# Kernel optimization log

Hardware: AMD Instinct MI355X
Metric: run time of the kernel (lower is better)

The kernel has to match this reference:

```python
import jax, jax.numpy as jnp
import numpy as np
import math

B, L, S, T = 16, 128, 128, 128
QDIM, FDIM, HID, ODIM = 512, 512, 512, 512

def setup_inputs() -> dict:
    key = jax.random.key(0)
    ks = jax.random.split(key, 9)
    sc = 0.02
    return {
        "query": jax.random.normal(ks[0], (B, L, QDIM), dtype=jnp.float32),
        "src": jax.random.normal(ks[1], (B, S, FDIM), dtype=jnp.float32),
        "trg": jax.random.normal(ks[2], (B, T, FDIM), dtype=jnp.float32),
        "Wq": jax.random.normal(ks[3], (QDIM, HID), dtype=jnp.float32) * sc,
        "bq": jnp.zeros((HID,), dtype=jnp.float32),
        "Ws": jax.random.normal(ks[4], (FDIM, HID), dtype=jnp.float32) * sc,
        "bs": jnp.zeros((HID,), dtype=jnp.float32),
        "Wo": jax.random.normal(ks[5], (FDIM * 2 + QDIM, ODIM), dtype=jnp.float32) * sc,
        "bo": jnp.zeros((ODIM,), dtype=jnp.float32),
    }

def reference(query, src, trg, Wq, bq, Ws, bs, Wo, bo):
    b, l, _ = query.shape
    s = src.shape[1]
    t = trg.shape[1]
    q = query @ Wq + bq            # [b,l,h]
    s_key = src @ Ws + bs          # [b,s,h]  (src_linear == trg_linear, shared weights)
    t_key = trg @ Ws + bs          # [b,t,h]
    # trilinear scores: [b,l,s,t]
    weight = jnp.einsum('blk,bsk,btk->blst', q, s_key, t_key) / math.sqrt(HID)
    weight = jax.nn.softmax(weight.reshape(b, l, s * t), axis=-1).reshape(b, l, s, t)
    s_ctx = jnp.einsum('blst,bsf->blf', weight, src)
    t_ctx = jnp.einsum('blst,btf->blf', weight, trg)
    x = jnp.concatenate((query, s_ctx, t_ctx), axis=-1)
    return x @ Wo + bo
```

## Files before the change

kernel.cpp:

```cpp
#include <hip/hip_runtime.h>
#include <hip/hip_bf16.h>

typedef __attribute__((ext_vector_type(8))) short short8;
typedef __attribute__((ext_vector_type(4))) short short4v;
typedef __attribute__((ext_vector_type(4))) float f32x4;
typedef __attribute__((ext_vector_type(8))) _Float16 half8;

#define DEVINL static __device__ __forceinline__

constexpr float SCORE_SCALE = 0.063758977414048896f;

typedef const __attribute__((address_space(1))) void gv_t;
typedef __attribute__((address_space(3))) void lv_t;
DEVINL void gload16(const void* g, void* l) {
  __builtin_amdgcn_global_load_lds((gv_t*)g, (lv_t*)l, 16, 0, 0);
}

#define SWZ_ADD(v, pat)                                                    \
  v += __int_as_float(__builtin_amdgcn_ds_swizzle(__float_as_int(v), pat))

template <int M, int N>
DEVINL void gemm16(const _Float16* A, const _Float16* B, int K, int lda, int ldb,
                   _Float16* ldsA, _Float16* ldsB, f32x4 acc[M / 32][N / 32])
{
  const int tid = threadIdx.x, lane = tid & 63;
  const int wr = (tid >> 7) & 1, wc = (tid >> 6) & 1;
  constexpr int MA = M / 32, NB = N / 32;
  int aoff[MA], boff[NB];
#pragma unroll
  for (int i = 0; i < MA; ++i) {
    const int ci = tid + i * 256, row = ci >> 3, c = ci & 7;
    aoff[i] = row * lda + ((c ^ (row & 7)) << 3);
  }
#pragma unroll
  for (int i = 0; i < NB; ++i) {
    const int ci = tid + i * 256, row = ci >> 3, c = ci & 7;
    boff[i] = row * ldb + ((c ^ (row & 7)) << 3);
  }
#define G16STAGE(cur, kk)                                                        \
  {                                                                              \
    _Pragma("unroll")                                                            \
    for (int i = 0; i < MA; ++i)                                                 \
      gload16(A + aoff[i] + (kk), ldsA + (cur) * (M * 64) + (tid + i * 256) * 8);\
    _Pragma("unroll")                                                            \
    for (int i = 0; i < NB; ++i)                                                 \
      gload16(B + boff[i] + (kk), ldsB + (cur) * (N * 64) + (tid + i * 256) * 8);\
  }
  G16STAGE(0, 0);
  __syncthreads();
  for (int kk = 0; kk < K; kk += 64) {
    const int cur = (kk >> 6) & 1;
    if (kk + 64 < K) G16STAGE(cur ^ 1, kk + 64);
    const _Float16* bA = ldsA + cur * (M * 64);
    const _Float16* bB = ldsB + cur * (N * 64);
#pragma unroll
    for (int s = 0; s < 2; ++s) {
      const int cg2 = s * 4 + (lane >> 4);
      half8 afr[MA], bfr[NB];
#pragma unroll
      for (int mi = 0; mi < MA; ++mi) {
        const int r = wr * (M / 2) + mi * 16 + (lane & 15);
        afr[mi] = *(const half8*)(bA + r * 64 + ((cg2 ^ (r & 7)) << 3));
      }
#pragma unroll
      for (int ni = 0; ni < NB; ++ni) {
        const int r = wc * (N / 2) + ni * 16 + (lane & 15);
        bfr[ni] = *(const half8*)(bB + r * 64 + ((cg2 ^ (r & 7)) << 3));
      }
#pragma unroll
      for (int mi = 0; mi < MA; ++mi)
#pragma unroll
        for (int ni = 0; ni < NB; ++ni)
          acc[mi][ni] = __builtin_amdgcn_mfma_f32_16x16x32_f16(afr[mi], bfr[ni], acc[mi][ni], 0, 0, 0);
    }
    __syncthreads();
  }
#undef G16STAGE
}

__global__ __launch_bounds__(256) void k_prep(
    const float* __restrict__ query, const float* __restrict__ src,
    const float* __restrict__ trg,
    const float* __restrict__ Wq, const float* __restrict__ Ws,
    const float* __restrict__ Wo,
    _Float16* __restrict__ qx, _Float16* __restrict__ srch,
    _Float16* __restrict__ trgh,
    _Float16* __restrict__ WqT, _Float16* __restrict__ WsT,
    _Float16* __restrict__ WoT)
{
  __shared__ float t[32][33];
  const int id = blockIdx.x, tid = threadIdx.x;
  if (id < 1536) {
    const int z = id >> 9;
    const int idx8 = (((id & 511) << 8) + tid) * 8;
    const float* in = (z == 0) ? query : (z == 1) ? src : trg;
    float4 va = *(const float4*)(in + idx8);
    float4 vb = *(const float4*)(in + idx8 + 4);
    half8 h;
    h[0] = (_Float16)va.x; h[1] = (_Float16)va.y;
    h[2] = (_Float16)va.z; h[3] = (_Float16)va.w;
    h[4] = (_Float16)vb.x; h[5] = (_Float16)vb.y;
    h[6] = (_Float16)vb.z; h[7] = (_Float16)vb.w;
    _Float16* o = (z == 0) ? qx : (z == 1) ? srch : trgh;
    *(half8*)(o + idx8) = h;
    return;
  }
  const float* in; _Float16* out; int KK, NN, bx, by;
  if (id < 1792)      { const int u = id - 1536; in = Wq; out = WqT; KK = 512;  NN = 512; bx = u & 15; by = u >> 4; }
  else if (id < 2048) { const int u = id - 1792; in = Ws; out = WsT; KK = 512;  NN = 512; bx = u & 15; by = u >> 4; }
  else                { const int u = id - 2048; in = Wo; out = WoT; KK = 1536; NN = 512; bx = u & 15; by = u >> 4; }
  const int tx = tid & 31, ty = tid >> 5;
  const int k0 = by * 32, n0 = bx * 32;
#pragma unroll
  for (int i = 0; i < 4; ++i)
    t[ty + i * 8][tx] = in[(size_t)(k0 + ty + i * 8) * NN + n0 + tx];
  __syncthreads();
#pragma unroll
  for (int i = 0; i < 4; ++i)
    out[(size_t)(n0 + ty + i * 8) * KK + k0 + tx] = (_Float16)t[tx][ty + i * 8];
}

__global__ __launch_bounds__(256) void k_proj(
    const _Float16* __restrict__ qx, const _Float16* __restrict__ srch,
    const _Float16* __restrict__ trgh,
    const _Float16* __restrict__ WqT, const _Float16* __restrict__ WsT,
    const _Float16* __restrict__ WoT,
    const float* __restrict__ bq, const float* __restrict__ bs,
    _Float16* __restrict__ qh, _Float16* __restrict__ skh,
    _Float16* __restrict__ tkh, _Float16* __restrict__ P2)
{
  __shared__ __align__(16) _Float16 lds[24576];
  const int id = blockIdx.x;
  const int tid = threadIdx.x, lane = tid & 63;
  const int wr = (tid >> 7) & 1, wc = (tid >> 6) & 1;
  const int r0 = wr * 32 + ((lane >> 4) << 2);
  const int c0 = wc * 64 + (lane & 15);

  f32x4 acc[2][4] = {};

  if (id < 384) {
    const int z = id >> 7, u = id & 127;
    const int bcol = (u & 3) * 128, brow = (u >> 2) * 64;
    const _Float16* A = (z == 0) ? qx : (z == 1) ? srch : trgh;
    const _Float16* BT = (z == 0) ? WqT : WsT;
    const float* bias = (z == 0) ? bq : bs;
    gemm16<64, 128>(A + (size_t)brow * 512, BT + (size_t)bcol * 512,
                    512, 512, 512, lds, lds + 8192, acc);
#pragma unroll
    for (int mi = 0; mi < 2; ++mi)
#pragma unroll
      for (int ni = 0; ni < 4; ++ni) {
        const int col = bcol + c0 + ni * 16;
        const float bv = bias[col];
#pragma unroll
        for (int r = 0; r < 4; ++r) {
          const int row = brow + r0 + mi * 16 + r;
          const float v = acc[mi][ni][r] + bv;
          if (z == 0)      qh[(size_t)row * 512 + col] = (_Float16)(v * SCORE_SCALE);
          else if (z == 1) skh[(size_t)row * 512 + col] = (_Float16)v;
          else             tkh[(size_t)row * 512 + col] = (_Float16)v;
        }
      }
  } else {
    const int side = (id - 384) >> 7, u = (id - 384) & 127;
    const int b = u >> 3, brow = (u & 7) * 64;
    const _Float16* A = WoT + (size_t)brow * 1536 + 512 + side * 512;
    const _Float16* B = (side ? trgh : srch) + (size_t)b * 65536;
    gemm16<64, 128>(A, B, 512, 1536, 512, lds, lds + 8192, acc);
    _Float16* P = P2 + (size_t)b * 131072 + side * 128;
#pragma unroll
    for (int mi = 0; mi < 2; ++mi)
#pragma unroll
      for (int ni = 0; ni < 4; ++ni) {
        const int col = c0 + ni * 16;
#pragma unroll
        for (int r = 0; r < 4; ++r) {
          const int row = brow + r0 + mi * 16 + r;
          P[(size_t)row * 256 + col] = (_Float16)acc[mi][ni][r];
        }
      }
  }
}

__global__ __launch_bounds__(512, 4) void k_score(
    const _Float16* __restrict__ qh, const _Float16* __restrict__ skh,
    const _Float16* __restrict__ tkh,
    _Float16* __restrict__ wct2)
{
  __shared__ __align__(16) char pool[51200];
  _Float16* qlds = (_Float16*)(pool + 49152);
  float* wsp   = (float*)(pool);
  float* wtp   = (float*)(pool + 4096);
  float* wfin  = (float*)(pool + 8192);
  float* denom = (float*)(pool + 12288);

  const int raw = blockIdx.x;
  const int swz = (raw & 7) * 128 + (raw >> 3);
  const int b = swz >> 6, l0 = (swz & 63) * 2;

  const int tid = threadIdx.x, lane = tid & 63, wid = tid >> 6;
  const int l = wid >> 2, qs = (wid >> 1) & 1, qt = wid & 1;
  const int cg = lane >> 4;
  const int ln = lane & 15;
  const _Float16* skb = skh + (size_t)b * 65536;
  const _Float16* tkb = tkh + (size_t)b * 65536;

  int soff;
  {
    const int row = tid >> 2, c = tid & 3;
    soff = row * 512 + ((c ^ ((row >> 1) & 3)) << 3);
  }

  if (tid < 256) {
    const int li = tid >> 7, e = (tid & 127) * 4;
    *(short4v*)(qlds + li * 512 + e) =
        *(const short4v*)(qh + (size_t)(b * 128 + l0 + li) * 512 + e);
  }

  const int rbase_s = (qs * 64 + ln) * 64;
  const int rbase_t = (qt * 64 + ln) * 64;
  const int sw = (cg ^ ((ln >> 1) & 3)) << 4;

#define KSTAGE(dstbuf, kt)                                                  \
  {                                                                         \
    gload16(skb + soff + (kt) * 32, (dstbuf) + tid * 16);                   \
    gload16(tkb + soff + (kt) * 32, (dstbuf) + 8192 + tid * 16);            \
  }

  f32x4 acc[4][4] = {};
  char* bufA = pool;
  char* bufB = pool + 16384;
  char* bufC = pool + 32768;
  KSTAGE(bufA, 0);
  KSTAGE(bufB, 1);
  asm volatile("s_waitcnt vmcnt(0) lgkmcnt(0)" ::: "memory");
  __builtin_amdgcn_sched_barrier(0);
  __builtin_amdgcn_s_barrier();
  __builtin_amdgcn_sched_barrier(0);

  for (int it = 0; it < 16; ++it) {
    if (it < 14) KSTAGE(bufC, it + 2);
    half8 qv = *(const half8*)(qlds + l * 512 + it * 32 + cg * 8);
    half8 sfr[4], tfr[4];
#pragma unroll
    for (int mi = 0; mi < 4; ++mi)
      sfr[mi] = *(const half8*)(bufA + rbase_s + mi * 1024 + sw);
#pragma unroll
    for (int ni = 0; ni < 4; ++ni)
      tfr[ni] = *(const half8*)(bufA + 8192 + rbase_t + ni * 1024 + sw);
    __builtin_amdgcn_s_setprio(1);
#pragma unroll
    for (int mi = 0; mi < 4; ++mi) {
      half8 a = sfr[mi] * qv;
#pragma unroll
      for (int ni = 0; ni < 4; ++ni)
        acc[mi][ni] = __builtin_amdgcn_mfma_f32_16x16x32_f16(a, tfr[ni], acc[mi][ni], 0, 0, 0);
    }
    __builtin_amdgcn_s_setprio(0);
    if (it < 14) { asm volatile("s_waitcnt vmcnt(2)" ::: "memory"); }
    else         { asm volatile("s_waitcnt vmcnt(0)" ::: "memory"); }
    __builtin_amdgcn_sched_barrier(0);
    __builtin_amdgcn_s_barrier();
    __builtin_amdgcn_sched_barrier(0);
    char* t_ = bufA; bufA = bufB; bufB = bufC; bufC = t_;
  }
#undef KSTAGE

#pragma unroll
  for (int mi = 0; mi < 4; ++mi)
#pragma unroll
    for (int ni = 0; ni < 4; ++ni)
#pragma unroll
      for (int r = 0; r < 4; ++r)
        acc[mi][ni][r] = exp2f(acc[mi][ni][r]);

#pragma unroll
  for (int mi = 0; mi < 4; ++mi)
#pragma unroll
    for (int r = 0; r < 4; ++r) {
      float v = acc[mi][0][r] + acc[mi][1][r] + acc[mi][2][r] + acc[mi][3][r];
      SWZ_ADD(v, 0x041F);
      SWZ_ADD(v, 0x081F);
      SWZ_ADD(v, 0x101F);
      SWZ_ADD(v, 0x201F);
      if ((lane & 15) == 0)
        wsp[(l * 2 + qt) * 128 + qs * 64 + mi * 16 + (lane >> 4) * 4 + r] = v;
    }
#pragma unroll
  for (int ni = 0; ni < 4; ++ni) {
    float v = 0.f;
#pragma unroll
    for (int mi = 0; mi < 4; ++mi)
#pragma unroll
      for (int r = 0; r < 4; ++r) v += acc[mi][ni][r];
    SWZ_ADD(v, 0x401F);
    v += __shfl_xor(v, 32);
    if (lane < 16) wtp[(l * 2 + qs) * 128 + qt * 64 + ni * 16 + lane] = v;
  }
  __syncthreads();

  if (tid < 256) {
    const int li = tid >> 7, idx = tid & 127;
    wfin[(li * 2 + 0) * 128 + idx] =
        wsp[(li * 2 + 0) * 128 + idx] + wsp[(li * 2 + 1) * 128 + idx];
  } else {
    const int u = tid - 256, li = u >> 7, idx = u & 127;
    wfin[(li * 2 + 1) * 128 + idx] =
        wtp[(li * 2 + 0) * 128 + idx] + wtp[(li * 2 + 1) * 128 + idx];
  }
  __syncthreads();
  if (wid < 2) {
    float v = wfin[wid * 256 + lane] + wfin[wid * 256 + lane + 64];
#pragma unroll
    for (int off = 32; off >= 1; off >>= 1) v += __shfl_xor(v, off);
    if (lane == 0) denom[wid] = v;
  }
  __syncthreads();
  const float inv0 = 1.0f / denom[0], inv1 = 1.0f / denom[1];

  if (tid < 256) {
    const int li = tid >> 7, idx = tid & 127;
    const float inv = li ? inv1 : inv0;
    wct2[((size_t)(b * 128 + l0 + li)) * 256 + idx] =
        (_Float16)(wfin[li * 256 + idx] * inv);
  } else {
    const int u = tid - 256, li = u >> 7, idx = u & 127;
    const float inv = li ? inv1 : inv0;
    wct2[((size_t)(b * 128 + l0 + li)) * 256 + 128 + idx] =
        (_Float16)(wfin[li * 256 + 128 + idx] * inv);
  }
}

__global__ __launch_bounds__(256) void k_final(
    const _Float16* __restrict__ qx, const _Float16* __restrict__ WoT,
    const _Float16* __restrict__ wct2, const _Float16* __restrict__ P2,
    const float* __restrict__ bo, float* __restrict__ out)
{
  __shared__ __align__(16) _Float16 lds[16384];
  const int brow = blockIdx.y * 64, bcol = blockIdx.x * 64;
  const int b = blockIdx.y >> 1;

  f32x4 acc[2][2] = {};
  gemm16<64, 64>(qx + (size_t)brow * 512, WoT + (size_t)bcol * 1536,
                 512, 512, 1536, lds, lds + 8192, acc);
  gemm16<64, 64>(wct2 + (size_t)brow * 256,
                 P2 + (size_t)b * 131072 + (size_t)bcol * 256,
                 256, 256, 256, lds, lds + 8192, acc);

  const int tid = threadIdx.x, lane = tid & 63;
  const int wr = (tid >> 7) & 1, wc = (tid >> 6) & 1;
  const int r0 = wr * 32 + ((lane >> 4) << 2);
  const int c0 = wc * 32 + (lane & 15);
#pragma unroll
  for (int mi = 0; mi < 2; ++mi)
#pragma unroll
    for (int ni = 0; ni < 2; ++ni) {
      const int col = bcol + c0 + ni * 16;
      const float bv = bo[col];
#pragma unroll
      for (int r = 0; r < 4; ++r) {
        const int row = brow + r0 + mi * 16 + r;
        out[(size_t)row * 512 + col] = acc[mi][ni][r] + bv;
      }
    }
}

extern "C" void kernel_launch(void* const* d_in, const int* in_sizes, int n_in,
                              void* d_out, int out_size, void* d_ws, size_t ws_size,
                              hipStream_t stream)
{
  (void)in_sizes; (void)n_in; (void)out_size; (void)ws_size;
  const float* query = (const float*)d_in[0];
  const float* src   = (const float*)d_in[1];
  const float* trg   = (const float*)d_in[2];
  const float* Wq    = (const float*)d_in[3];
  const float* bq    = (const float*)d_in[4];
  const float* Ws    = (const float*)d_in[5];
  const float* bs    = (const float*)d_in[6];
  const float* Wo    = (const float*)d_in[7];
  const float* bo    = (const float*)d_in[8];
  float* out = (float*)d_out;

  char* w = (char*)d_ws;
  _Float16* qx   = (_Float16*)(w);
  _Float16* qh   = (_Float16*)(w + (2u  << 20));
  _Float16* skh  = (_Float16*)(w + (4u  << 20));
  _Float16* tkh  = (_Float16*)(w + (6u  << 20));
  _Float16* srch = (_Float16*)(w + (8u  << 20));
  _Float16* trgh = (_Float16*)(w + (10u << 20));
  _Float16* WqT  = (_Float16*)(w + (12u << 20));
  _Float16* WsT  = (_Float16*)(w + (13u << 20));
  _Float16* WoT  = (_Float16*)(w + (14u << 20));
  _Float16* wct2 = (_Float16*)(w + (16u << 20));
  _Float16* P2   = (_Float16*)(w + (17u << 20));

  k_prep<<<2816, 256, 0, stream>>>(query, src, trg, Wq, Ws, Wo,
                                   qx, srch, trgh, WqT, WsT, WoT);
  k_proj<<<640, 256, 0, stream>>>(qx, srch, trgh, WqT, WsT, WoT, bq, bs,
                                  qh, skh, tkh, P2);
  k_score<<<1024, 512, 0, stream>>>(qh, skh, tkh, wct2);
  k_final<<<dim3(8, 32), 256, 0, stream>>>(qx, WoT, wct2, P2, bo, out);
}
```

Measured before the change: 70.52 us.

## Deepen score kernel pipeline to four LDS stages with register double-buffering

The score kernel's K-loop moves from a three-buffer LDS ring to a four-buffer ring, prefetching three stages ahead. It is fully unrolled with two alternating register fragment sets, so LDS reads for the next step are issued before the current step's MFMAs, overlapping LDS latency with matrix math. Shared memory grows to about 66 KB and launch bounds drop from 4 to 2 blocks per SM. Occupancy may fall as a result, and register pressure rises from the duplicate fragment sets.

```diff
diff --git a/kernel.cpp b/kernel.cpp
--- a/kernel.cpp
+++ b/kernel.cpp
@@ -182,13 +182,13 @@
   }
 }
 
-__global__ __launch_bounds__(512, 4) void k_score(
+__global__ __launch_bounds__(512, 2) void k_score(
     const _Float16* __restrict__ qh, const _Float16* __restrict__ skh,
     const _Float16* __restrict__ tkh,
     _Float16* __restrict__ wct2)
 {
-  __shared__ __align__(16) char pool[51200];
-  _Float16* qlds = (_Float16*)(pool + 49152);
+  __shared__ __align__(16) char pool[67584];
+  _Float16* qlds = (_Float16*)(pool + 65536);
   float* wsp   = (float*)(pool);
   float* wtp   = (float*)(pool + 4096);
   float* wfin  = (float*)(pool + 8192);
@@ -221,49 +221,80 @@
   const int rbase_t = (qt * 64 + ln) * 64;
   const int sw = (cg ^ ((ln >> 1) & 3)) << 4;
 
-#define KSTAGE(dstbuf, kt)                                                  \
+#define KSTAGE(bufidx, kt)                                                  \
   {                                                                         \
-    gload16(skb + soff + (kt) * 32, (dstbuf) + tid * 16);                   \
-    gload16(tkb + soff + (kt) * 32, (dstbuf) + 8192 + tid * 16);            \
-  }
-
+    char* d_ = pool + (bufidx) * 16384;                                     \
+    gload16(skb + soff + (kt) * 32, d_ + tid * 16);                         \
+    gload16(tkb + soff + (kt) * 32, d_ + 8192 + tid * 16);                  \
+  }
+
+  half8 sfrA[4], tfrA[4], qvA;
+  half8 sfrB[4], tfrB[4], qvB;
   f32x4 acc[4][4] = {};
-  char* bufA = pool;
-  char* bufB = pool + 16384;
-  char* bufC = pool + 32768;
-  KSTAGE(bufA, 0);
-  KSTAGE(bufB, 1);
+
+#define PRELOAD(SET, bufidx, itn)                                           \
+  {                                                                         \
+    const char* S_ = pool + (bufidx) * 16384;                               \
+    const char* T_ = S_ + 8192;                                             \
+    _Pragma("unroll")                                                       \
+    for (int mi = 0; mi < 4; ++mi)                                          \
+      sfr##SET[mi] = *(const half8*)(S_ + rbase_s + mi * 1024 + sw);        \
+    _Pragma("unroll")                                                       \
+    for (int ni = 0; ni < 4; ++ni)                                          \
+      tfr##SET[ni] = *(const half8*)(T_ + rbase_t + ni * 1024 + sw);        \
+    qv##SET = *(const half8*)(qlds + l * 512 + (itn) * 32 + cg * 8);        \
+  }
+
+#define MFMAPH(SET)                                                         \
+  {                                                                         \
+    __builtin_amdgcn_s_setprio(1);                                          \
+    _Pragma("unroll")                                                       \
+    for (int mi = 0; mi < 4; ++mi) {                                        \
+      half8 a = sfr##SET[mi] * qv##SET;                                     \
+      _Pragma("unroll")                                                     \
+      for (int ni = 0; ni < 4; ++ni)                                        \
+        acc[mi][ni] = __builtin_amdgcn_mfma_f32_16x16x32_f16(a, tfr##SET[ni], acc[mi][ni], 0, 0, 0); \
+    }                                                                       \
+    __builtin_amdgcn_s_setprio(0);                                          \
+  }
+
+#define ITER(i, X, Y)                                                       \
+  {                                                                         \
+    if ((i) < 13) KSTAGE(((i) + 3) & 3, (i) + 3);                           \
+    if ((i) < 15) {                                                         \
+      PRELOAD(Y, ((i) + 1) & 3, (i) + 1);                                   \
+      asm volatile("s_waitcnt lgkmcnt(9)" ::: "memory");                    \
+    } else {                                                                \
+      asm volatile("s_waitcnt lgkmcnt(0)" ::: "memory");                    \
+    }                                                                       \
+    __builtin_amdgcn_sched_barrier(0);                                      \
+    MFMAPH(X);                                                              \
+    if ((i) < 15) {                                                         \
+      if ((i) < 13) { asm volatile("s_waitcnt vmcnt(2)" ::: "memory"); }    \
+      else          { asm volatile("s_waitcnt vmcnt(0)" ::: "memory"); }    \
+      __builtin_amdgcn_sched_barrier(0);                                    \
+      __builtin_amdgcn_s_barrier();                                         \
+      __builtin_amdgcn_sched_barrier(0);                                    \
+    }                                                                       \
+  }
+
+  KSTAGE(0, 0);
+  KSTAGE(1, 1);
+  KSTAGE(2, 2);
   asm volatile("s_waitcnt vmcnt(0) lgkmcnt(0)" ::: "memory");
   __builtin_amdgcn_sched_barrier(0);
   __builtin_amdgcn_s_barrier();
   __builtin_amdgcn_sched_barrier(0);
-
-  for (int it = 0; it < 16; ++it) {
-    if (it < 14) KSTAGE(bufC, it + 2);
-    half8 qv = *(const half8*)(qlds + l * 512 + it * 32 + cg * 8);
-    half8 sfr[4], tfr[4];
-#pragma unroll
-    for (int mi = 0; mi < 4; ++mi)
-      sfr[mi] = *(const half8*)(bufA + rbase_s + mi * 1024 + sw);
-#pragma unroll
-    for (int ni = 0; ni < 4; ++ni)
-      tfr[ni] = *(const half8*)(bufA + 8192 + rbase_t + ni * 1024 + sw);
-    __builtin_amdgcn_s_setprio(1);
-#pragma unroll
-    for (int mi = 0; mi < 4; ++mi) {
-      half8 a = sfr[mi] * qv;
-#pragma unroll
-      for (int ni = 0; ni < 4; ++ni)
-        acc[mi][ni] = __builtin_amdgcn_mfma_f32_16x16x32_f16(a, tfr[ni], acc[mi][ni], 0, 0, 0);
-    }
-    __builtin_amdgcn_s_setprio(0);
-    if (it < 14) { asm volatile("s_waitcnt vmcnt(2)" ::: "memory"); }
-    else         { asm volatile("s_waitcnt vmcnt(0)" ::: "memory"); }
-    __builtin_amdgcn_sched_barrier(0);
-    __builtin_amdgcn_s_barrier();
-    __builtin_amdgcn_sched_barrier(0);
-    char* t_ = bufA; bufA = bufB; bufB = bufC; bufC = t_;
-  }
+  PRELOAD(A, 0, 0);
+
+  ITER(0, A, B)  ITER(1, B, A)  ITER(2, A, B)  ITER(3, B, A)
+  ITER(4, A, B)  ITER(5, B, A)  ITER(6, A, B)  ITER(7, B, A)
+  ITER(8, A, B)  ITER(9, B, A)  ITER(10, A, B) ITER(11, B, A)
+  ITER(12, A, B) ITER(13, B, A) ITER(14, A, B) ITER(15, B, A)
+
+#undef ITER
+#undef MFMAPH
+#undef PRELOAD
 #undef KSTAGE
 
 #pragma unroll
```

Measured after the change: 78.87 us. 11.8% more time.
